# Kernel tuning notes

Measured on AMD Instinct MI355X. Metric: run time of the kernel, lower is better.

The kernel has to match this reference:

```python
import jax, jax.numpy as jnp
import numpy as np

WIN_LENGTH = 2048
HOP_LENGTH = 512
N_FRAMES = 16384
FFT_SIZE = WIN_LENGTH // 2 + 1  # 1025 frequency bins


def _gl_alg(window_size, hop, fft_size):
    """Griffin-Lim ideal synthesis window (numpy, static precompute)."""
    syn_w = np.hamming(window_size) / np.sqrt(fft_size)  # scipy.signal.hamming == np.hamming (sym)
    syn_w_prod = syn_w ** 2.0
    redundancy = int(window_size / hop)
    env = np.zeros(window_size)
    for k in range(-redundancy, redundancy + 1):
        win_ind = np.arange(1, window_size + 1)
        env_ind = hop * k + win_ind
        valid = (env_ind > 0) & (env_ind <= window_size)
        env[env_ind[valid] - 1] += syn_w_prod[win_ind[valid] - 1]
    return syn_w / env


def setup_inputs() -> dict:
    key = jax.random.key(0)
    k1, k2 = jax.random.split(key)
    magnitude = jax.random.uniform(k1, (N_FRAMES, FFT_SIZE), dtype=jnp.float32)
    phase = jax.random.normal(k2, (N_FRAMES, FFT_SIZE), dtype=jnp.float32)
    return {"magnitude": magnitude, "phase": phase}


def reference(magnitude, phase):
    win, hop = WIN_LENGTH, HOP_LENGTH
    T, F = magnitude.shape
    fft_points = (F - 1) * 2          # 2048-point IFFT
    hw_1 = (win + 1) // 2
    hw_2 = win // 2

    # static synthesis window (matches _gl_alg(win_length, hop, (win_length-1)*2))
    rs = jnp.asarray(_gl_alg(win, hop, (win - 1) * 2), dtype=magnitude.dtype)

    # Hermitian-symmetric spectrum + real(ifft) == irfft (imag of DC/Nyquist ignored)
    spec = jax.lax.complex(magnitude * jnp.cos(phase), magnitude * jnp.sin(phase))  # [T, F]
    fft_buf = jnp.fft.irfft(spec, n=fft_points, axis=-1)  # [T, fft_points], real

    # fftshift-style rearrangement into a win_length frame
    y = jnp.concatenate([fft_buf[:, -hw_2:], fft_buf[:, :hw_1]], axis=-1) * rs

    # windowed overlap-add via scatter-add (fold)
    L = T * hop + hw_1 + hw_2
    idx = (jnp.arange(T)[:, None] * hop + jnp.arange(win)[None, :]).reshape(-1)
    sig = jnp.zeros((L,), dtype=y.dtype).at[idx].add(y.reshape(-1))

    # trim transients: first 3*hop samples and last 3*hop+1 samples
    return sig[3 * hop : L - (3 * hop + 1)]
```

## Files before the change

### kernel.cpp

```cpp
#include <hip/hip_runtime.h>

#define WIN      2048
#define HOP      512
#define NFRAMES  16384
#define NBINS    1025
#define FPB      16

__device__ __forceinline__ int pidx(int a) { return a + (a >> 3); }
__device__ __forceinline__ float2 cmul(float2 a, float2 b) {
    return make_float2(a.x * b.x - a.y * b.y, a.x * b.y + a.y * b.x);
}

__global__ __launch_bounds__(256, 4) void istft_kernel(
        const float* __restrict__ mag, const float* __restrict__ ph,
        float* __restrict__ out, int out_size) {
    __shared__ float2 W1[1152];
    __shared__ float2 W2[1152];
    __shared__ float2 S0[1026], S1[1026];

    const int tid    = threadIdx.x;
    const int frame0 = blockIdx.x * FPB;

    float2 wpk;
    sincospif((float)tid * (1.0f / 1024.0f), &wpk.y, &wpk.x);
    float2 wst[4], w2st[4];
    wst[0] = cmul(wpk, wpk);
    sincospif((float)(tid & ~3)  * (1.0f / 512.0f), &wst[1].y, &wst[1].x);
    sincospif((float)(tid & ~15) * (1.0f / 512.0f), &wst[2].y, &wst[2].x);
    sincospif((float)(tid & ~63) * (1.0f / 512.0f), &wst[3].y, &wst[3].x);
    #pragma unroll
    for (int q = 0; q < 4; ++q) w2st[q] = cmul(wst[q], wst[q]);

    float2 rq[4];
    {
        const float inv2047 = 1.0f / 2047.0f;
        const float scale   = rsqrtf(4094.0f);
        float he[4], ho[4];
        float envE = 0.0f, envO = 0.0f;
        #pragma unroll
        for (int w = 0; w < 4; ++w) {
            he[w] = (0.54f - 0.46f * cospif((float)(2 * tid     + 512 * w) * 2.0f * inv2047)) * scale;
            ho[w] = (0.54f - 0.46f * cospif((float)(2 * tid + 1 + 512 * w) * 2.0f * inv2047)) * scale;
            envE += he[w] * he[w];
            envO += ho[w] * ho[w];
        }
        const float se = 1.0f / (envE * 1024.0f);
        const float so = 1.0f / (envO * 1024.0f);
        #pragma unroll
        for (int w = 0; w < 4; ++w) rq[w] = make_float2(he[w] * se, ho[w] * so);
    }
    const float2 r0 = rq[0], r1 = rq[1], r2 = rq[2], r3 = rq[3];
    const float RT = 0.70710678118654752f;

    float2 xkA0, xkA1, xkA2, xkA3;
    float2 xkB0, xkB1, xkB2, xkB3;
    float  mgn[4], ppn[4], nymg, nyph;
    float2 acc0, acc1, acc2, acc3;
    acc0 = acc1 = acc2 = acc3 = make_float2(0.0f, 0.0f);
    float2* Scur = S0;
    float2* Snxt = S1;

    {
        const float* magf = mag + (size_t)frame0 * NBINS;
        const float* phf  = ph  + (size_t)frame0 * NBINS;
        #pragma unroll
        for (int j = 0; j < 4; ++j) {
            mgn[j] = magf[tid + 256 * j];
            ppn[j] = phf[tid + 256 * j];
        }
        nymg = magf[1024]; nyph = phf[1024];
        float2 X[4];
        #pragma unroll
        for (int j = 0; j < 4; ++j) {
            float s, c;
            __sincosf(ppn[j], &s, &c);
            X[j] = make_float2(mgn[j] * c, mgn[j] * s);
            if (j == 0 && tid == 0) X[j].y = 0.0f;
            Scur[tid + 256 * j] = X[j];
        }
        xkA0 = X[0]; xkA1 = X[1]; xkA2 = X[2]; xkA3 = X[3];
        if (tid == 0) {
            float s, c;
            __sincosf(nyph, &s, &c);
            Scur[1024] = make_float2(nymg * c, 0.0f);
        }
    }
    __syncthreads();

    for (int fi = 0; fi < FPB; ++fi) {
        if (fi < FPB - 1) {
            const float* magf = mag + (size_t)(frame0 + fi + 1) * NBINS;
            const float* phf  = ph  + (size_t)(frame0 + fi + 1) * NBINS;
            #pragma unroll
            for (int j = 0; j < 4; ++j) {
                mgn[j] = magf[tid + 256 * j];
                ppn[j] = phf[tid + 256 * j];
            }
            nymg = magf[1024]; nyph = phf[1024];
        }
        {
            float2 z[4];
            #pragma unroll
            for (int j = 0; j < 4; ++j) {
                float2 Xk = (j == 0) ? xkA0 : (j == 1) ? xkA1 : (j == 2) ? xkA2 : xkA3;
                float2 Xm = Scur[1024 - (tid + 256 * j)];
                float2 wj;
                if      (j == 0) wj = wpk;
                else if (j == 1) wj = make_float2(RT * (wpk.x - wpk.y), RT * (wpk.x + wpk.y));
                else if (j == 2) wj = make_float2(-wpk.y, wpk.x);
                else             wj = make_float2(-RT * (wpk.x + wpk.y), RT * (wpk.x - wpk.y));
                float Er = 0.5f * (Xk.x + Xm.x), Ei = 0.5f * (Xk.y - Xm.y);
                float Tr = Xm.x - Xk.x,          Ti = -Xm.y - Xk.y;
                float Or = 0.5f * (wj.x * Ti + wj.y * Tr);
                float Oi = 0.5f * (wj.y * Ti - wj.x * Tr);
                z[j] = make_float2(Er + Or, Ei + Oi);
            }
            float2 w = wst[0], w2 = w2st[0];
            float2 u0 = make_float2(z[0].x + z[2].x, z[0].y + z[2].y);
            float  ar = z[0].x - z[2].x, ai = z[0].y - z[2].y;
            float2 u1 = make_float2(ar * w.x - ai * w.y, ar * w.y + ai * w.x);
            float2 u2 = make_float2(z[1].x + z[3].x, z[1].y + z[3].y);
            float  br = z[1].x - z[3].x, bi = z[1].y - z[3].y;
            float2 u3 = make_float2(-br * w.y - bi * w.x, br * w.x - bi * w.y);
            const int base = 4 * tid;
            W1[pidx(base)]     = make_float2(u0.x + u2.x, u0.y + u2.y);
            W1[pidx(base + 1)] = make_float2(u1.x + u3.x, u1.y + u3.y);
            float dr = u0.x - u2.x, di = u0.y - u2.y;
            W1[pidx(base + 2)] = make_float2(dr * w2.x - di * w2.y, dr * w2.y + di * w2.x);
            float er = u1.x - u3.x, ei = u1.y - u3.y;
            W1[pidx(base + 3)] = make_float2(er * w2.x - ei * w2.y, er * w2.y + ei * w2.x);
        }
        __syncthreads();

        #pragma unroll
        for (int st = 1; st < 4; ++st) {
            float2* src = (st == 2) ? W2 : W1;
            float2* dst = (st == 2) ? W1 : W2;
            const int s4 = 1 << (2 * st);
            const int G  = tid & ~(s4 - 1);
            const float2 w = wst[st], w2 = w2st[st];
            float2 x0 = src[pidx(tid)];
            float2 x1 = src[pidx(tid + 256)];
            float2 x2 = src[pidx(tid + 512)];
            float2 x3 = src[pidx(tid + 768)];
            float2 u0 = make_float2(x0.x + x2.x, x0.y + x2.y);
            float  ar = x0.x - x2.x, ai = x0.y - x2.y;
            float2 u1 = make_float2(ar * w.x - ai * w.y, ar * w.y + ai * w.x);
            float2 u2 = make_float2(x1.x + x3.x, x1.y + x3.y);
            float  br = x1.x - x3.x, bi = x1.y - x3.y;
            float2 u3 = make_float2(-br * w.y - bi * w.x, br * w.x - bi * w.y);
            const int base = tid + 3 * G;
            dst[pidx(base)]          = make_float2(u0.x + u2.x, u0.y + u2.y);
            dst[pidx(base + s4)]     = make_float2(u1.x + u3.x, u1.y + u3.y);
            float dr = u0.x - u2.x, di = u0.y - u2.y;
            dst[pidx(base + 2 * s4)] = make_float2(dr * w2.x - di * w2.y, dr * w2.y + di * w2.x);
            float er = u1.x - u3.x, ei = u1.y - u3.y;
            dst[pidx(base + 3 * s4)] = make_float2(er * w2.x - ei * w2.y, er * w2.y + ei * w2.x);

            if (st == 3 && fi < FPB - 1) {
                float2 X[4];
                #pragma unroll
                for (int j = 0; j < 4; ++j) {
                    float s, c;
                    __sincosf(ppn[j], &s, &c);
                    X[j] = make_float2(mgn[j] * c, mgn[j] * s);
                    if (j == 0 && tid == 0) X[j].y = 0.0f;
                    Snxt[tid + 256 * j] = X[j];
                }
                xkB0 = X[0]; xkB1 = X[1]; xkB2 = X[2]; xkB3 = X[3];
                if (tid == 0) {
                    float s, c;
                    __sincosf(nyph, &s, &c);
                    Snxt[1024] = make_float2(nymg * c, 0.0f);
                }
            }
            __syncthreads();
        }

        {
            float2 x0 = W2[pidx(tid)];
            float2 x1 = W2[pidx(tid + 256)];
            float2 x2 = W2[pidx(tid + 512)];
            float2 x3 = W2[pidx(tid + 768)];
            float2 u0 = make_float2(x0.x + x2.x, x0.y + x2.y);
            float2 u1 = make_float2(x0.x - x2.x, x0.y - x2.y);
            float2 u2 = make_float2(x1.x + x3.x, x1.y + x3.y);
            float2 u3 = make_float2(-(x1.y - x3.y), x1.x - x3.x);
            float2 y;
            y = make_float2(u0.x - u2.x, u0.y - u2.y);
            acc0.x += y.x * r0.x;  acc0.y += y.y * r0.y;
            y = make_float2(u1.x - u3.x, u1.y - u3.y);
            acc1.x += y.x * r1.x;  acc1.y += y.y * r1.y;
            y = make_float2(u0.x + u2.x, u0.y + u2.y);
            acc2.x += y.x * r2.x;  acc2.y += y.y * r2.y;
            y = make_float2(u1.x + u3.x, u1.y + u3.y);
            acc3.x += y.x * r3.x;  acc3.y += y.y * r3.y;

            float2 v = acc0;
            long p = (long)(frame0 + fi) * HOP + 2 * tid - 1536;
            if (fi >= 3) {
                if (p >= 0 && p < out_size)         out[p]     = v.x;
                if (p + 1 >= 0 && p + 1 < out_size) out[p + 1] = v.y;
            } else {
                if (p >= 0 && p < out_size)         atomicAdd(out + p,     v.x);
                if (p + 1 >= 0 && p + 1 < out_size) atomicAdd(out + p + 1, v.y);
            }
            acc0 = acc1; acc1 = acc2; acc2 = acc3;
            acc3 = make_float2(0.0f, 0.0f);
            xkA0 = xkB0; xkA1 = xkB1; xkA2 = xkB2; xkA3 = xkB3;
            float2* tmp = Scur; Scur = Snxt; Snxt = tmp;
        }
    }

    #pragma unroll
    for (int e = 0; e < 3; ++e) {
        float2 v = (e == 0) ? acc0 : (e == 1) ? acc1 : acc2;
        long p = (long)(frame0 + FPB + e) * HOP + 2 * tid - 1536;
        if (p >= 0 && p < out_size)         atomicAdd(out + p,     v.x);
        if (p + 1 >= 0 && p + 1 < out_size) atomicAdd(out + p + 1, v.y);
    }
}

extern "C" void kernel_launch(void* const* d_in, const int* in_sizes, int n_in,
                              void* d_out, int out_size, void* d_ws, size_t ws_size,
                              hipStream_t stream) {
    const float* mag = (const float*)d_in[0];
    const float* ph  = (const float*)d_in[1];
    float* out = (float*)d_out;

    hipMemsetAsync(d_out, 0, (size_t)out_size * sizeof(float), stream);
    istft_kernel<<<NFRAMES / FPB, 256, 0, stream>>>(mag, ph, out, out_size);
}
```

Before: 58.22 us.

## Pair mirrored bins via wave shuffles, drop spectrum LDS buffers, halve frames per block

Threads now own bins b and their mirrors 1024-b inside the same wavefront, so the Hermitian pairing is done with xor-63 lane shuffles instead of a double-buffered spectrum array in shared memory. That removes the S0/S1 LDS arrays and their stores and loads. Frames per block drop from 16 to 8 and launch bounds rise to 8 waves per SIMD, so occupancy goes up. In exchange, the extra blocks mean more boundary frames handled with atomicAdd, and the sincos work is no longer overlapped with the FFT stages.

```diff
diff --git a/kernel.cpp b/kernel.cpp
--- a/kernel.cpp
+++ b/kernel.cpp
@@ -4,32 +4,38 @@
 #define HOP      512
 #define NFRAMES  16384
 #define NBINS    1025
-#define FPB      16
+#define FPB      8
 
 __device__ __forceinline__ int pidx(int a) { return a + (a >> 3); }
 __device__ __forceinline__ float2 cmul(float2 a, float2 b) {
     return make_float2(a.x * b.x - a.y * b.y, a.x * b.y + a.y * b.x);
 }
-
-__global__ __launch_bounds__(256, 4) void istft_kernel(
+__device__ __forceinline__ float2 shfl63(float2 v) {
+    return make_float2(__shfl_xor(v.x, 63, 64), __shfl_xor(v.y, 63, 64));
+}
+
+__global__ __launch_bounds__(256, 8) void istft_kernel(
         const float* __restrict__ mag, const float* __restrict__ ph,
         float* __restrict__ out, int out_size) {
     __shared__ float2 W1[1152];
     __shared__ float2 W2[1152];
-    __shared__ float2 S0[1026], S1[1026];
 
     const int tid    = threadIdx.x;
     const int frame0 = blockIdx.x * FPB;
-
-    float2 wpk;
-    sincospif((float)tid * (1.0f / 1024.0f), &wpk.y, &wpk.x);
-    float2 wst[4], w2st[4];
-    wst[0] = cmul(wpk, wpk);
+    const int l  = tid & 63;
+    const int wv = tid >> 6;
+    int bm = (l < 32) ? (32 * wv + l) : (193 - 32 * wv + l);
+    if (tid == 63) bm = 128;
+    const int b = bm;
+
+    float2 wpb;
+    sincospif((float)b * (1.0f / 1024.0f), &wpb.y, &wpb.x);
+    const float2 w0 = cmul(wpb, wpb);
+    float2 wst[4];
+    wst[0] = w0;
     sincospif((float)(tid & ~3)  * (1.0f / 512.0f), &wst[1].y, &wst[1].x);
     sincospif((float)(tid & ~15) * (1.0f / 512.0f), &wst[2].y, &wst[2].x);
     sincospif((float)(tid & ~63) * (1.0f / 512.0f), &wst[3].y, &wst[3].x);
-    #pragma unroll
-    for (int q = 0; q < 4; ++q) w2st[q] = cmul(wst[q], wst[q]);
 
     float2 rq[4];
     {
@@ -52,77 +58,72 @@
     const float2 r0 = rq[0], r1 = rq[1], r2 = rq[2], r3 = rq[3];
     const float RT = 0.70710678118654752f;
 
-    float2 xkA0, xkA1, xkA2, xkA3;
-    float2 xkB0, xkB1, xkB2, xkB3;
     float  mgn[4], ppn[4], nymg, nyph;
     float2 acc0, acc1, acc2, acc3;
     acc0 = acc1 = acc2 = acc3 = make_float2(0.0f, 0.0f);
-    float2* Scur = S0;
-    float2* Snxt = S1;
 
     {
         const float* magf = mag + (size_t)frame0 * NBINS;
         const float* phf  = ph  + (size_t)frame0 * NBINS;
         #pragma unroll
-        for (int j = 0; j < 4; ++j) {
-            mgn[j] = magf[tid + 256 * j];
-            ppn[j] = phf[tid + 256 * j];
+        for (int m = 0; m < 4; ++m) {
+            mgn[m] = magf[256 * m + b];
+            ppn[m] = phf[256 * m + b];
         }
         nymg = magf[1024]; nyph = phf[1024];
-        float2 X[4];
-        #pragma unroll
-        for (int j = 0; j < 4; ++j) {
+    }
+
+    for (int fi = 0; fi < FPB; ++fi) {
+        float2 X0, X1, X2, X3, Xn;
+        {
             float s, c;
-            __sincosf(ppn[j], &s, &c);
-            X[j] = make_float2(mgn[j] * c, mgn[j] * s);
-            if (j == 0 && tid == 0) X[j].y = 0.0f;
-            Scur[tid + 256 * j] = X[j];
-        }
-        xkA0 = X[0]; xkA1 = X[1]; xkA2 = X[2]; xkA3 = X[3];
-        if (tid == 0) {
-            float s, c;
-            __sincosf(nyph, &s, &c);
-            Scur[1024] = make_float2(nymg * c, 0.0f);
-        }
-    }
-    __syncthreads();
-
-    for (int fi = 0; fi < FPB; ++fi) {
+            __sincosf(ppn[0], &s, &c); X0 = make_float2(mgn[0] * c, mgn[0] * s);
+            __sincosf(ppn[1], &s, &c); X1 = make_float2(mgn[1] * c, mgn[1] * s);
+            __sincosf(ppn[2], &s, &c); X2 = make_float2(mgn[2] * c, mgn[2] * s);
+            __sincosf(ppn[3], &s, &c); X3 = make_float2(mgn[3] * c, mgn[3] * s);
+            __sincosf(nyph,   &s, &c); Xn = make_float2(nymg * c, 0.0f);
+        }
+        if (b == 0) X0.y = 0.0f;
+        float2 Xm0 = shfl63(X3), Xm1 = shfl63(X2), Xm2 = shfl63(X1), Xm3 = shfl63(X0);
+        if (b == 0)   { Xm0 = Xn; Xm1 = X3; Xm2 = X2; Xm3 = X1; }
+        if (b == 128) { Xm0 = X3; Xm1 = X2; Xm2 = X1; Xm3 = X0; }
+
         if (fi < FPB - 1) {
             const float* magf = mag + (size_t)(frame0 + fi + 1) * NBINS;
             const float* phf  = ph  + (size_t)(frame0 + fi + 1) * NBINS;
             #pragma unroll
-            for (int j = 0; j < 4; ++j) {
-                mgn[j] = magf[tid + 256 * j];
-                ppn[j] = phf[tid + 256 * j];
+            for (int m = 0; m < 4; ++m) {
+                mgn[m] = magf[256 * m + b];
+                ppn[m] = phf[256 * m + b];
             }
             nymg = magf[1024]; nyph = phf[1024];
         }
+
         {
             float2 z[4];
             #pragma unroll
-            for (int j = 0; j < 4; ++j) {
-                float2 Xk = (j == 0) ? xkA0 : (j == 1) ? xkA1 : (j == 2) ? xkA2 : xkA3;
-                float2 Xm = Scur[1024 - (tid + 256 * j)];
-                float2 wj;
-                if      (j == 0) wj = wpk;
-                else if (j == 1) wj = make_float2(RT * (wpk.x - wpk.y), RT * (wpk.x + wpk.y));
-                else if (j == 2) wj = make_float2(-wpk.y, wpk.x);
-                else             wj = make_float2(-RT * (wpk.x + wpk.y), RT * (wpk.x - wpk.y));
+            for (int m = 0; m < 4; ++m) {
+                float2 Xk = (m == 0) ? X0 : (m == 1) ? X1 : (m == 2) ? X2 : X3;
+                float2 Xm = (m == 0) ? Xm0 : (m == 1) ? Xm1 : (m == 2) ? Xm2 : Xm3;
+                float2 tp;
+                if      (m == 0) tp = wpb;
+                else if (m == 1) tp = make_float2(RT * (wpb.x - wpb.y), RT * (wpb.x + wpb.y));
+                else if (m == 2) tp = make_float2(-wpb.y, wpb.x);
+                else             tp = make_float2(-RT * (wpb.x + wpb.y), RT * (wpb.x - wpb.y));
                 float Er = 0.5f * (Xk.x + Xm.x), Ei = 0.5f * (Xk.y - Xm.y);
-                float Tr = Xm.x - Xk.x,          Ti = -Xm.y - Xk.y;
-                float Or = 0.5f * (wj.x * Ti + wj.y * Tr);
-                float Oi = 0.5f * (wj.y * Ti - wj.x * Tr);
-                z[j] = make_float2(Er + Or, Ei + Oi);
+                float Tr = Xm.x - Xk.x,          Ti = -(Xm.y + Xk.y);
+                float Or = 0.5f * (tp.x * Ti + tp.y * Tr);
+                float Oi = 0.5f * (tp.y * Ti - tp.x * Tr);
+                z[m] = make_float2(Er + Or, Ei + Oi);
             }
-            float2 w = wst[0], w2 = w2st[0];
+            const float2 w = w0, w2 = cmul(w0, w0);
             float2 u0 = make_float2(z[0].x + z[2].x, z[0].y + z[2].y);
             float  ar = z[0].x - z[2].x, ai = z[0].y - z[2].y;
             float2 u1 = make_float2(ar * w.x - ai * w.y, ar * w.y + ai * w.x);
             float2 u2 = make_float2(z[1].x + z[3].x, z[1].y + z[3].y);
             float  br = z[1].x - z[3].x, bi = z[1].y - z[3].y;
             float2 u3 = make_float2(-br * w.y - bi * w.x, br * w.x - bi * w.y);
-            const int base = 4 * tid;
+            const int base = 4 * b;
             W1[pidx(base)]     = make_float2(u0.x + u2.x, u0.y + u2.y);
             W1[pidx(base + 1)] = make_float2(u1.x + u3.x, u1.y + u3.y);
             float dr = u0.x - u2.x, di = u0.y - u2.y;
@@ -138,7 +139,8 @@
             float2* dst = (st == 2) ? W1 : W2;
             const int s4 = 1 << (2 * st);
             const int G  = tid & ~(s4 - 1);
-            const float2 w = wst[st], w2 = w2st[st];
+            const float2 w = wst[st];
+            const float2 w2 = cmul(w, w);
             float2 x0 = src[pidx(tid)];
             float2 x1 = src[pidx(tid + 256)];
             float2 x2 = src[pidx(tid + 512)];
@@ -156,24 +158,6 @@
             dst[pidx(base + 2 * s4)] = make_float2(dr * w2.x - di * w2.y, dr * w2.y + di * w2.x);
             float er = u1.x - u3.x, ei = u1.y - u3.y;
             dst[pidx(base + 3 * s4)] = make_float2(er * w2.x - ei * w2.y, er * w2.y + ei * w2.x);
-
-            if (st == 3 && fi < FPB - 1) {
-                float2 X[4];
-                #pragma unroll
-                for (int j = 0; j < 4; ++j) {
-                    float s, c;
-                    __sincosf(ppn[j], &s, &c);
-                    X[j] = make_float2(mgn[j] * c, mgn[j] * s);
-                    if (j == 0 && tid == 0) X[j].y = 0.0f;
-                    Snxt[tid + 256 * j] = X[j];
-                }
-                xkB0 = X[0]; xkB1 = X[1]; xkB2 = X[2]; xkB3 = X[3];
-                if (tid == 0) {
-                    float s, c;
-                    __sincosf(nyph, &s, &c);
-                    Snxt[1024] = make_float2(nymg * c, 0.0f);
-                }
-            }
             __syncthreads();
         }
 
@@ -207,8 +191,6 @@
             }
             acc0 = acc1; acc1 = acc2; acc2 = acc3;
             acc3 = make_float2(0.0f, 0.0f);
-            xkA0 = xkB0; xkA1 = xkB1; xkA2 = xkB2; xkA3 = xkB3;
-            float2* tmp = Scur; Scur = Snxt; Snxt = tmp;
         }
     }
 
```

New measurement: 208.8 us. +258.6%, slower.
